# Performance work log

Measured on AMD Instinct MI355X. Metric: run time of the kernel, lower is better.

Reference implementation:

```python
import jax, jax.numpy as jnp
import numpy as np

LATENT = 256; INPUT = 128; NUNITS = 256; DEC_OUT = 128
NTRAJ = 256; NTP = 512
INTERP = 2  # hard-coded in the original forward

def _mlp_sig(x, w1, b1, w2, b2):
    return jax.nn.sigmoid(jnp.tanh(x @ w1 + b1) @ w2 + b2)

def _mlp_lin(x, w1, b1, w2, b2):
    return jnp.tanh(x @ w1 + b1) @ w2 + b2

def _gru_step(y, yt, x, ug, ugt, rg, ns):
    # x: [N, 2*INPUT]; first half = features, second half = observation mask channels
    xh = x[:, :INPUT]
    yc = jnp.concatenate([y, xh], axis=-1)                 # [N, LATENT+INPUT]
    u = _mlp_sig(yc, *ug)
    ut = _mlp_sig(yc, *ugt)
    r = _mlp_sig(yc, *rg)
    new_state = _mlp_lin(jnp.concatenate([y * r, xh], axis=-1), *ns)
    new_y = (1.0 - u) * new_state + u * y
    new_yt = (1.0 - ut) * new_state + ut * yt
    mask = (jnp.sum(x[:, INPUT:], axis=-1, keepdims=True) > 0).astype(x.dtype)
    return mask * new_y + (1.0 - mask) * y, mask * new_yt + (1.0 - mask) * yt

def setup_inputs():
    key = jax.random.key(0)
    ks = iter(jax.random.split(key, 32))
    def p(shape):
        return jax.random.normal(next(ks), shape, dtype=jnp.float32) * 0.05
    d = {}
    d["data"] = jax.random.normal(next(ks), (NTRAJ, NTP, 2 * INPUT), dtype=jnp.float32)
    dts = jax.random.uniform(next(ks), (NTRAJ, NTP), dtype=jnp.float32) + 0.1
    d["time_steps"] = jnp.cumsum(dts, axis=1)              # strictly increasing times
    gin = LATENT + INPUT
    for name in ("ug", "ugt", "rg", "rgt", "ns"):
        d[name + "_w1"] = p((gin, NUNITS)); d[name + "_b1"] = jnp.zeros((NUNITS,), jnp.float32)
        d[name + "_w2"] = p((NUNITS, LATENT)); d[name + "_b2"] = jnp.zeros((LATENT,), jnp.float32)
    d["dk_w1"] = p((LATENT, LATENT)); d["dk_b1"] = jnp.zeros((LATENT,), jnp.float32)
    d["dk_w2"] = p((LATENT, 1)); d["dk_b2"] = jnp.zeros((1,), jnp.float32)
    d["dec_w"] = p((LATENT, DEC_OUT)); d["dec_b"] = jnp.zeros((DEC_OUT,), jnp.float32)
    return d

def reference(data, time_steps,
              ug_w1, ug_b1, ug_w2, ug_b2,
              ugt_w1, ugt_b1, ugt_w2, ugt_b2,
              rg_w1, rg_b1, rg_w2, rg_b2,
              rgt_w1, rgt_b1, rgt_w2, rgt_b2,
              ns_w1, ns_b1, ns_w2, ns_b2,
              dk_w1, dk_b1, dk_w2, dk_b2,
              dec_w, dec_b):
    # Note: reset_gate_target (rgt_*) is computed but never used in the original forward.
    ug = (ug_w1, ug_b1, ug_w2, ug_b2)
    ugt = (ugt_w1, ugt_b1, ugt_w2, ugt_b2)
    rg = (rg_w1, rg_b1, rg_w2, rg_b2)
    ns = (ns_w1, ns_b1, ns_w2, ns_b2)
    n_traj = data.shape[0]
    lin = jnp.linspace(0.0, 1.0, INTERP + 1, dtype=data.dtype)  # [3]
    y0 = jnp.zeros((n_traj, LATENT), data.dtype)
    # step i=0: no decay interpolation, yi_decay = prev_y (zeros)
    y, yt = _gru_step(y0, y0, data[:, 0, :], ug, ugt, rg, ns)
    dts = time_steps[:, 1:] - time_steps[:, :-1]                # [N, T-1]
    xs = jnp.moveaxis(data[:, 1:, :], 1, 0)                     # [T-1, N, 2I]

    def step(carry, inp):
        y, yt = carry
        x, dt = inp
        decay = jax.nn.relu(jax.nn.relu(y @ dk_w1 + dk_b1) @ dk_w2 + dk_b2)  # [N,1]
        e = jnp.exp(-decay * (dt[:, None] * lin[None, :]))                   # [N,3]
        ydec = yt[:, None, :] + (y - yt)[:, None, :] * e[:, :, None]         # [N,3,L]
        vol = jnp.mean(ydec[:, :-1, :] @ dec_w + dec_b, axis=-2)             # [N,D]
        y2, yt2 = _gru_step(ydec[:, -1, :], yt, x, ug, ugt, rg, ns)
        return (y2, yt2), vol

    (y, yt), vols = jax.lax.scan(step, (y, yt), (xs, dts.T))
    prev_y = y[None, :, :]                       # [1, N, L]
    volume_dt = jnp.transpose(vols, (1, 0, 2))   # [N, T-1, D]
    return prev_y, volume_dt, dts
```

## Files before the change

### kernel.cpp

```cpp
#include <hip/hip_runtime.h>
#include <hip/hip_fp16.h>

#define NTRAJ   256
#define NTP     512
#define NSTEPS  511
#define LATENT  256
#define INPUT   128
#define DEC_OUT 128

#define OUT_VOL ((size_t)NTRAJ * LATENT)
#define OUT_DTS (OUT_VOL + (size_t)NTRAJ * NSTEPS * DEC_OUT)

#define WU_UG1  0
#define WU_UG2  49152
#define WU_UGT1 81920
#define WU_UGT2 131072
#define WU_RG1  163840
#define WU_RG2  212992
#define WU_NS1  245760
#define WU_NS2  294912
#define WU_DK1  327680
#define WU_DEC  360448
#define WU_TOT  376832

typedef _Float16 h2_t __attribute__((ext_vector_type(2)));
union U32H2 { unsigned int u; h2_t h; };

__device__ __forceinline__ float dot2f(unsigned int wu, unsigned int xu, float acc) {
#if defined(__has_builtin) && __has_builtin(__builtin_amdgcn_fdot2)
    U32H2 a, b; a.u = wu; b.u = xu;
    return __builtin_amdgcn_fdot2(a.h, b.h, acc, false);
#else
    U32H2 a, b; a.u = wu; b.u = xu;
    return acc + (float)a.h.x * (float)b.h.x + (float)a.h.y * (float)b.h.y;
#endif
}

__device__ __forceinline__ float wred(float v) {
    #pragma unroll
    for (int off = 32; off; off >>= 1) v += __shfl_down(v, off, 64);
    return v;
}
__device__ __forceinline__ float fast_sigmoid(float x) { return 1.0f / (1.0f + __expf(-x)); }
__device__ __forceinline__ float fast_tanh(float x) {
    float e = __expf(2.0f * x);
    return 1.0f - 2.0f / (e + 1.0f);
}
__device__ __forceinline__ unsigned int packpair(float v) {
    float vn = __shfl_xor(v, 1, 64);
    U32H2 r; r.h.x = (_Float16)v; r.h.y = (_Float16)vn;
    return r.u;
}

extern "C" __global__ void __launch_bounds__(256)
convert_w(const float* __restrict__ ug_w1, const float* __restrict__ ug_w2,
          const float* __restrict__ ugt_w1, const float* __restrict__ ugt_w2,
          const float* __restrict__ rg_w1, const float* __restrict__ rg_w2,
          const float* __restrict__ ns_w1, const float* __restrict__ ns_w2,
          const float* __restrict__ dk_w1, const float* __restrict__ dec_w,
          unsigned int* __restrict__ ws)
{
    const int i = blockIdx.x * 256 + threadIdx.x;
    const float* s; int o; int cbits;
    if      (i < WU_UG2)  { s = ug_w1;  o = i;           cbits = 8; }
    else if (i < WU_UGT1) { s = ug_w2;  o = i - WU_UG2;  cbits = 8; }
    else if (i < WU_UGT2) { s = ugt_w1; o = i - WU_UGT1; cbits = 8; }
    else if (i < WU_RG1)  { s = ugt_w2; o = i - WU_UGT2; cbits = 8; }
    else if (i < WU_RG2)  { s = rg_w1;  o = i - WU_RG1;  cbits = 8; }
    else if (i < WU_NS1)  { s = rg_w2;  o = i - WU_RG2;  cbits = 8; }
    else if (i < WU_NS2)  { s = ns_w1;  o = i - WU_NS1;  cbits = 8; }
    else if (i < WU_DK1)  { s = ns_w2;  o = i - WU_NS2;  cbits = 8; }
    else if (i < WU_DEC)  { s = dk_w1;  o = i - WU_DK1;  cbits = 8; }
    else                  { s = dec_w;  o = i - WU_DEC;  cbits = 7; }
    const int C  = 1 << cbits;
    const int kp = o >> cbits;
    const int c  = o & (C - 1);
    const float v0 = s[(2 * kp) * C + c];
    const float v1 = s[(2 * kp + 1) * C + c];
    const unsigned int h0 = __half_as_ushort(__float2half(v0));
    const unsigned int h1 = __half_as_ushort(__float2half(v1));
    ws[i] = h0 | (h1 << 16);
}

#define DOT1(acc, wv, xv) { \
    acc.x = dot2f((wv).x, (xv), acc.x); acc.y = dot2f((wv).y, (xv), acc.y); \
    acc.z = dot2f((wv).z, (xv), acc.z); acc.w = dot2f((wv).w, (xv), acc.w); }

extern "C" __global__ void __launch_bounds__(1024, 4)
rnn_decay_kernel7(const float* __restrict__ data, const float* __restrict__ ts,
                  const float* __restrict__ ug_b1, const float* __restrict__ ug_b2,
                  const float* __restrict__ ugt_b1, const float* __restrict__ ugt_b2,
                  const float* __restrict__ rg_b1, const float* __restrict__ rg_b2,
                  const float* __restrict__ ns_b1, const float* __restrict__ ns_b2,
                  const float* __restrict__ dk_b1, const float* __restrict__ dk_w2,
                  const float* __restrict__ dk_b2, const float* __restrict__ dec_b,
                  const unsigned int* __restrict__ wsu, float* __restrict__ out)
{
    __shared__ __align__(16) float s_part[12288];
    __shared__ __align__(16) float s_partd[4096];
    __shared__ __align__(16) unsigned int s_in_h[192];
    __shared__ __align__(16) unsigned int s_ns_h[192];
    __shared__ __align__(16) unsigned int s_y_h[128];
    __shared__ __align__(16) unsigned int s_a_h[128];
    __shared__ __align__(16) unsigned int s_b_h[128];
    __shared__ __align__(16) unsigned int s_c_h[128];
    __shared__ __align__(16) unsigned int s_v_h[128];
    __shared__ float s_ut[256];
    __shared__ float s_red[8];

    const int tid  = threadIdx.x;
    const int w    = tid >> 6;
    const int lane = tid & 63;
    const int c    = tid & 255;
    const int cl4  = lane << 2;
    const int traj = blockIdx.x;

    const unsigned int* UG1  = wsu + WU_UG1;  const unsigned int* UG2  = wsu + WU_UG2;
    const unsigned int* UGT1 = wsu + WU_UGT1; const unsigned int* UGT2 = wsu + WU_UGT2;
    const unsigned int* RG1  = wsu + WU_RG1;  const unsigned int* RG2  = wsu + WU_RG2;
    const unsigned int* NS1  = wsu + WU_NS1;  const unsigned int* NS2  = wsu + WU_NS2;
    const unsigned int* DK1  = wsu + WU_DK1;  const unsigned int* DECW = wsu + WU_DEC;

    const float* dbase = data + (size_t)traj * NTP * (2 * INPUT);
    const float* tbase = ts + (size_t)traj * NTP;
    float* vol_out = out + OUT_VOL + (size_t)traj * NSTEPS * DEC_OUT;
    float* dts_out = out + OUT_DTS + (size_t)traj * NSTEPS;

    if (tid < 256)
        for (int t0 = c; t0 < NSTEPS; t0 += 256)
            dts_out[t0] = tbase[t0 + 1] - tbase[t0];

    float r_y = 0.f, r_yt = 0.f;

    const int kp12 = w * 12;
    const int kp8  = w << 3;

    for (int t = -1; t < NSTEPS; ++t) {
        const bool first = (t < 0);

        if (tid < 256) {
            const float xval = first ? dbase[c] : dbase[(size_t)(t + 1) * 256 + c];
            float mv = (c >= 128) ? xval : 0.f;
            mv = wred(mv);
            if (lane == 0) s_red[w] = mv;
            if (c < 128) {
                const unsigned int px = packpair(xval);
                if (!(lane & 1)) { s_in_h[128 + (c >> 1)] = px; s_ns_h[128 + (c >> 1)] = px; }
            }
            if (first && !(lane & 1)) s_in_h[c >> 1] = 0u;
        }

        float r_ydec = 0.f, r_u = 0.f;
        bool maskv;

        if (!first) {
            {
                float4 aD = make_float4(0.f, 0.f, 0.f, 0.f);
                #pragma unroll 4
                for (int i = 0; i < 8; ++i) {
                    const int kp = kp8 + i;
                    const unsigned int xv = s_y_h[kp];
                    const uint4 wv = *(const uint4*)(DK1 + (size_t)kp * 256 + cl4);
                    DOT1(aD, wv, xv);
                }
                *(float4*)(s_part + (w << 8) + cl4) = aD;
            }
            __syncthreads();
            if (tid < 256) {
                float v = dk_b1[c];
                #pragma unroll
                for (int i = 0; i < 16; ++i) v += s_part[(i << 8) + c];
                v = fmaxf(v, 0.f);
                const float pv = wred(v * dk_w2[c]);
                if (lane == 0) s_red[4 + w] = pv;
            }
            __syncthreads();
            maskv = (s_red[0] + s_red[1] + s_red[2] + s_red[3]) > 0.f;
            if (tid < 256) {
                const float decay = fmaxf(s_red[4] + s_red[5] + s_red[6] + s_red[7]
                                        + dk_b2[0], 0.f);
                const float dt = tbase[t + 1] - tbase[t];
                const float diff = r_y - r_yt;
                const float ef = __expf(-decay * dt);
                const float eh = __expf(-0.5f * decay * dt);
                r_ydec = r_yt + diff * ef;
                const float vol = 0.5f * (r_y + r_yt + diff * eh);
                const unsigned int pd  = packpair(r_ydec);
                const unsigned int pvv = packpair(vol);
                if (!(lane & 1)) { s_in_h[c >> 1] = pd; s_v_h[c >> 1] = pvv; }
            }
            __syncthreads();
        } else {
            __syncthreads();
            maskv = (s_red[0] + s_red[1] + s_red[2] + s_red[3]) > 0.f;
        }

        if (!first) {
            float4 aE = make_float4(0.f, 0.f, 0.f, 0.f);
            const int hh = lane >> 5, cl = (lane & 31) << 2;
            const int kpb = kp8 + hh;
            #pragma unroll
            for (int i = 0; i < 4; ++i) {
                const int kp = kpb + (i << 1);
                const uint4 wv = *(const uint4*)(DECW + (size_t)kp * 128 + cl);
                const unsigned int xv = s_v_h[kp];
                DOT1(aE, wv, xv);
            }
            *(float4*)(s_partd + ((w << 1) + hh) * 128 + cl) = aE;
        }

        {
            float4 aA = make_float4(0.f, 0.f, 0.f, 0.f), aB = aA, aC = aA;
            #pragma unroll 4
            for (int i = 0; i < 12; ++i) {
                const int kp = kp12 + i;
                const unsigned int xv = s_in_h[kp];
                const uint4 wa = *(const uint4*)(UG1  + (size_t)kp * 256 + cl4);
                const uint4 wb = *(const uint4*)(UGT1 + (size_t)kp * 256 + cl4);
                const uint4 wc = *(const uint4*)(RG1  + (size_t)kp * 256 + cl4);
                DOT1(aA, wa, xv); DOT1(aB, wb, xv); DOT1(aC, wc, xv);
            }
            *(float4*)(s_part + (w << 8) + cl4)          = aA;
            *(float4*)(s_part + 4096 + (w << 8) + cl4)   = aB;
            *(float4*)(s_part + 8192 + (w << 8) + cl4)   = aC;
        }
        __syncthreads();
        {
            const int s = tid >> 8;
            if (s == 0) {
                float v = ug_b1[c];
                #pragma unroll
                for (int i = 0; i < 16; ++i) v += s_part[(i << 8) + c];
                v = fast_tanh(v);
                const unsigned int pk = packpair(v);
                if (!(lane & 1)) s_a_h[c >> 1] = pk;
            } else if (s == 1) {
                float v = ugt_b1[c];
                #pragma unroll
                for (int i = 0; i < 16; ++i) v += s_part[4096 + (i << 8) + c];
                v = fast_tanh(v);
                const unsigned int pk = packpair(v);
                if (!(lane & 1)) s_b_h[c >> 1] = pk;
            } else if (s == 2) {
                float v = rg_b1[c];
                #pragma unroll
                for (int i = 0; i < 16; ++i) v += s_part[8192 + (i << 8) + c];
                v = fast_tanh(v);
                const unsigned int pk = packpair(v);
                if (!(lane & 1)) s_c_h[c >> 1] = pk;
            } else if (!first && c < 128) {
                float vd = dec_b[c];
                #pragma unroll
                for (int i = 0; i < 32; ++i) vd += s_partd[(i << 7) + c];
                vol_out[(size_t)t * DEC_OUT + c] = vd;
            }
        }
        __syncthreads();

        {
            float4 aA = make_float4(0.f, 0.f, 0.f, 0.f), aB = aA, aC = aA;
            #pragma unroll 4
            for (int i = 0; i < 8; ++i) {
                const int kp = kp8 + i;
                const unsigned int xa = s_a_h[kp];
                const unsigned int xb = s_b_h[kp];
                const unsigned int xc = s_c_h[kp];
                const uint4 wa = *(const uint4*)(UG2  + (size_t)kp * 256 + cl4);
                const uint4 wb = *(const uint4*)(UGT2 + (size_t)kp * 256 + cl4);
                const uint4 wc = *(const uint4*)(RG2  + (size_t)kp * 256 + cl4);
                DOT1(aA, wa, xa); DOT1(aB, wb, xb); DOT1(aC, wc, xc);
            }
            *(float4*)(s_part + (w << 8) + cl4)          = aA;
            *(float4*)(s_part + 4096 + (w << 8) + cl4)   = aB;
            *(float4*)(s_part + 8192 + (w << 8) + cl4)   = aC;
        }
        __syncthreads();
        {
            const int s = tid >> 8;
            if (s == 0) {
                float v = ug_b2[c];
                #pragma unroll
                for (int i = 0; i < 16; ++i) v += s_part[(i << 8) + c];
                r_u = fast_sigmoid(v);
                float v2 = rg_b2[c];
                #pragma unroll
                for (int i = 0; i < 16; ++i) v2 += s_part[8192 + (i << 8) + c];
                const float rr = fast_sigmoid(v2);
                const unsigned int pk = packpair(r_ydec * rr);
                if (!(lane & 1)) s_ns_h[c >> 1] = pk;
            } else if (s == 1) {
                float v = ugt_b2[c];
                #pragma unroll
                for (int i = 0; i < 16; ++i) v += s_part[4096 + (i << 8) + c];
                s_ut[c] = fast_sigmoid(v);
            }
        }
        __syncthreads();

        {
            float4 aA = make_float4(0.f, 0.f, 0.f, 0.f);
            #pragma unroll 4
            for (int i = 0; i < 12; ++i) {
                const int kp = kp12 + i;
                const unsigned int xv = s_ns_h[kp];
                const uint4 wa = *(const uint4*)(NS1 + (size_t)kp * 256 + cl4);
                DOT1(aA, wa, xv);
            }
            *(float4*)(s_part + (w << 8) + cl4) = aA;
        }
        __syncthreads();
        if (tid < 256) {
            float v = ns_b1[c];
            #pragma unroll
            for (int i = 0; i < 16; ++i) v += s_part[(i << 8) + c];
            v = fast_tanh(v);
            const unsigned int pk = packpair(v);
            if (!(lane & 1)) s_a_h[c >> 1] = pk;
        }
        __syncthreads();

        {
            float4 aA = make_float4(0.f, 0.f, 0.f, 0.f);
            #pragma unroll 4
            for (int i = 0; i < 8; ++i) {
                const int kp = kp8 + i;
                const unsigned int xv = s_a_h[kp];
                const uint4 wa = *(const uint4*)(NS2 + (size_t)kp * 256 + cl4);
                DOT1(aA, wa, xv);
            }
            *(float4*)(s_part + (w << 8) + cl4) = aA;
        }
        __syncthreads();
        if (tid < 256) {
            float nsv = ns_b2[c];
            #pragma unroll
            for (int i = 0; i < 16; ++i) nsv += s_part[(i << 8) + c];
            const float u = r_u, ut = s_ut[c];
            const float ny  = (1.f - u)  * nsv + u  * r_ydec;
            const float nyt = (1.f - ut) * nsv + ut * r_yt;
            r_y  = maskv ? ny  : r_ydec;
            r_yt = maskv ? nyt : r_yt;
            const unsigned int pk = packpair(r_y);
            if (!(lane & 1)) s_y_h[c >> 1] = pk;
        }
        __syncthreads();
    }

    if (tid < 256)
        out[(size_t)traj * 256 + c] = r_y;
}

extern "C" void kernel_launch(void* const* d_in, const int* in_sizes, int n_in,
                              void* d_out, int out_size, void* d_ws, size_t ws_size,
                              hipStream_t stream) {
    const float* data   = (const float*)d_in[0];
    const float* ts     = (const float*)d_in[1];
    const float* ug_w1  = (const float*)d_in[2];
    const float* ug_b1  = (const float*)d_in[3];
    const float* ug_w2  = (const float*)d_in[4];
    const float* ug_b2  = (const float*)d_in[5];
    const float* ugt_w1 = (const float*)d_in[6];
    const float* ugt_b1 = (const float*)d_in[7];
    const float* ugt_w2 = (const float*)d_in[8];
    const float* ugt_b2 = (const float*)d_in[9];
    const float* rg_w1  = (const float*)d_in[10];
    const float* rg_b1  = (const float*)d_in[11];
    const float* rg_w2  = (const float*)d_in[12];
    const float* rg_b2  = (const float*)d_in[13];
    const float* ns_w1  = (const float*)d_in[18];
    const float* ns_b1  = (const float*)d_in[19];
    const float* ns_w2  = (const float*)d_in[20];
    const float* ns_b2  = (const float*)d_in[21];
    const float* dk_w1  = (const float*)d_in[22];
    const float* dk_b1  = (const float*)d_in[23];
    const float* dk_w2  = (const float*)d_in[24];
    const float* dk_b2  = (const float*)d_in[25];
    const float* dec_w  = (const float*)d_in[26];
    const float* dec_b  = (const float*)d_in[27];

    unsigned int* wsu = (unsigned int*)d_ws;

    convert_w<<<WU_TOT / 256, 256, 0, stream>>>(ug_w1, ug_w2, ugt_w1, ugt_w2,
                                                rg_w1, rg_w2, ns_w1, ns_w2,
                                                dk_w1, dec_w, wsu);

    rnn_decay_kernel7<<<NTRAJ, 1024, 0, stream>>>(
        data, ts, ug_b1, ug_b2, ugt_b1, ugt_b2, rg_b1, rg_b2, ns_b1, ns_b2,
        dk_b1, dk_w2, dk_b2, dec_b, wsu, (float*)d_out);
}
```

Measured before the change: 7.624 ms.

## Process two trajectories per block to share weight loads across trajectories

```diff
diff --git a/kernel.cpp b/kernel.cpp
--- a/kernel.cpp
+++ b/kernel.cpp
@@ -86,8 +86,8 @@
     acc.x = dot2f((wv).x, (xv), acc.x); acc.y = dot2f((wv).y, (xv), acc.y); \
     acc.z = dot2f((wv).z, (xv), acc.z); acc.w = dot2f((wv).w, (xv), acc.w); }
 
-extern "C" __global__ void __launch_bounds__(1024, 4)
-rnn_decay_kernel7(const float* __restrict__ data, const float* __restrict__ ts,
+extern "C" __global__ void __launch_bounds__(512, 2)
+rnn_decay_kernel8(const float* __restrict__ data, const float* __restrict__ ts,
                   const float* __restrict__ ug_b1, const float* __restrict__ ug_b2,
                   const float* __restrict__ ugt_b1, const float* __restrict__ ugt_b2,
                   const float* __restrict__ rg_b1, const float* __restrict__ rg_b2,
@@ -96,24 +96,24 @@
                   const float* __restrict__ dk_b2, const float* __restrict__ dec_b,
                   const unsigned int* __restrict__ wsu, float* __restrict__ out)
 {
-    __shared__ __align__(16) float s_part[12288];
-    __shared__ __align__(16) float s_partd[4096];
-    __shared__ __align__(16) unsigned int s_in_h[192];
-    __shared__ __align__(16) unsigned int s_ns_h[192];
-    __shared__ __align__(16) unsigned int s_y_h[128];
-    __shared__ __align__(16) unsigned int s_a_h[128];
-    __shared__ __align__(16) unsigned int s_b_h[128];
-    __shared__ __align__(16) unsigned int s_c_h[128];
-    __shared__ __align__(16) unsigned int s_v_h[128];
-    __shared__ float s_ut[256];
-    __shared__ float s_red[8];
+    __shared__ __align__(16) float s_part[2][8192];
+    __shared__ __align__(16) unsigned int s_in_h[2][192];
+    __shared__ __align__(16) unsigned int s_ns_h[2][192];
+    __shared__ __align__(16) unsigned int s_y_h[2][128];
+    __shared__ __align__(16) unsigned int s_a_h[2][128];
+    __shared__ __align__(16) unsigned int s_b_h[2][128];
+    __shared__ __align__(16) unsigned int s_c_h[2][128];
+    __shared__ __align__(16) unsigned int s_v_h[2][128];
+    __shared__ float s_red[2][8];
 
     const int tid  = threadIdx.x;
     const int w    = tid >> 6;
     const int lane = tid & 63;
     const int c    = tid & 255;
+    const int h    = tid >> 8;
+    const int wg   = w & 3;
     const int cl4  = lane << 2;
-    const int traj = blockIdx.x;
+    const int traj = (blockIdx.x << 1) + h;
 
     const unsigned int* UG1  = wsu + WU_UG1;  const unsigned int* UG2  = wsu + WU_UG2;
     const unsigned int* UGT1 = wsu + WU_UGT1; const unsigned int* UGT2 = wsu + WU_UGT2;
@@ -126,59 +126,60 @@
     float* vol_out = out + OUT_VOL + (size_t)traj * NSTEPS * DEC_OUT;
     float* dts_out = out + OUT_DTS + (size_t)traj * NSTEPS;
 
-    if (tid < 256)
-        for (int t0 = c; t0 < NSTEPS; t0 += 256)
-            dts_out[t0] = tbase[t0 + 1] - tbase[t0];
+    for (int t0 = c; t0 < NSTEPS; t0 += 256)
+        dts_out[t0] = tbase[t0 + 1] - tbase[t0];
 
     float r_y = 0.f, r_yt = 0.f;
 
-    const int kp12 = w * 12;
-    const int kp8  = w << 3;
+    const int kp24 = w * 24;
+    const int kp16 = w << 4;
 
     for (int t = -1; t < NSTEPS; ++t) {
         const bool first = (t < 0);
 
-        if (tid < 256) {
+        {
             const float xval = first ? dbase[c] : dbase[(size_t)(t + 1) * 256 + c];
             float mv = (c >= 128) ? xval : 0.f;
             mv = wred(mv);
-            if (lane == 0) s_red[w] = mv;
+            if (lane == 0) s_red[h][wg] = mv;
             if (c < 128) {
                 const unsigned int px = packpair(xval);
-                if (!(lane & 1)) { s_in_h[128 + (c >> 1)] = px; s_ns_h[128 + (c >> 1)] = px; }
-            }
-            if (first && !(lane & 1)) s_in_h[c >> 1] = 0u;
-        }
-
-        float r_ydec = 0.f, r_u = 0.f;
+                if (!(lane & 1)) { s_in_h[h][128 + (c >> 1)] = px; s_ns_h[h][128 + (c >> 1)] = px; }
+            }
+            if (first && !(lane & 1)) s_in_h[h][c >> 1] = 0u;
+        }
+
+        float r_ydec = 0.f, r_u = 0.f, r_ut = 0.f;
         bool maskv;
 
         if (!first) {
             {
-                float4 aD = make_float4(0.f, 0.f, 0.f, 0.f);
+                float4 a0 = make_float4(0.f, 0.f, 0.f, 0.f), a1 = a0;
                 #pragma unroll 4
-                for (int i = 0; i < 8; ++i) {
-                    const int kp = kp8 + i;
-                    const unsigned int xv = s_y_h[kp];
+                for (int i = 0; i < 16; ++i) {
+                    const int kp = kp16 + i;
+                    const unsigned int x0 = s_y_h[0][kp];
+                    const unsigned int x1 = s_y_h[1][kp];
                     const uint4 wv = *(const uint4*)(DK1 + (size_t)kp * 256 + cl4);
-                    DOT1(aD, wv, xv);
+                    DOT1(a0, wv, x0); DOT1(a1, wv, x1);
                 }
-                *(float4*)(s_part + (w << 8) + cl4) = aD;
+                *(float4*)(&s_part[0][(w << 8) + cl4]) = a0;
+                *(float4*)(&s_part[1][(w << 8) + cl4]) = a1;
             }
             __syncthreads();
-            if (tid < 256) {
+            {
                 float v = dk_b1[c];
                 #pragma unroll
-                for (int i = 0; i < 16; ++i) v += s_part[(i << 8) + c];
+                for (int i = 0; i < 8; ++i) v += s_part[h][(i << 8) + c];
                 v = fmaxf(v, 0.f);
                 const float pv = wred(v * dk_w2[c]);
-                if (lane == 0) s_red[4 + w] = pv;
+                if (lane == 0) s_red[h][4 + wg] = pv;
             }
             __syncthreads();
-            maskv = (s_red[0] + s_red[1] + s_red[2] + s_red[3]) > 0.f;
-            if (tid < 256) {
-                const float decay = fmaxf(s_red[4] + s_red[5] + s_red[6] + s_red[7]
-                                        + dk_b2[0], 0.f);
+            maskv = (s_red[h][0] + s_red[h][1] + s_red[h][2] + s_red[h][3]) > 0.f;
+            {
+                const float decay = fmaxf(s_red[h][4] + s_red[h][5] + s_red[h][6]
+                                        + s_red[h][7] + dk_b2[0], 0.f);
                 const float dt = tbase[t + 1] - tbase[t];
                 const float diff = r_y - r_yt;
                 const float ef = __expf(-decay * dt);
@@ -187,167 +188,177 @@
                 const float vol = 0.5f * (r_y + r_yt + diff * eh);
                 const unsigned int pd  = packpair(r_ydec);
                 const unsigned int pvv = packpair(vol);
-                if (!(lane & 1)) { s_in_h[c >> 1] = pd; s_v_h[c >> 1] = pvv; }
+                if (!(lane & 1)) { s_in_h[h][c >> 1] = pd; s_v_h[h][c >> 1] = pvv; }
             }
             __syncthreads();
         } else {
             __syncthreads();
-            maskv = (s_red[0] + s_red[1] + s_red[2] + s_red[3]) > 0.f;
+            maskv = (s_red[h][0] + s_red[h][1] + s_red[h][2] + s_red[h][3]) > 0.f;
         }
 
         if (!first) {
-            float4 aE = make_float4(0.f, 0.f, 0.f, 0.f);
+            float4 e0 = make_float4(0.f, 0.f, 0.f, 0.f), e1 = e0;
             const int hh = lane >> 5, cl = (lane & 31) << 2;
-            const int kpb = kp8 + hh;
-            #pragma unroll
-            for (int i = 0; i < 4; ++i) {
+            const int kpb = kp16 + hh;
+            #pragma unroll 4
+            for (int i = 0; i < 8; ++i) {
                 const int kp = kpb + (i << 1);
                 const uint4 wv = *(const uint4*)(DECW + (size_t)kp * 128 + cl);
-                const unsigned int xv = s_v_h[kp];
-                DOT1(aE, wv, xv);
-            }
-            *(float4*)(s_partd + ((w << 1) + hh) * 128 + cl) = aE;
-        }
-
-        {
-            float4 aA = make_float4(0.f, 0.f, 0.f, 0.f), aB = aA, aC = aA;
+                const unsigned int x0 = s_v_h[0][kp];
+                const unsigned int x1 = s_v_h[1][kp];
+                DOT1(e0, wv, x0); DOT1(e1, wv, x1);
+            }
+            const int slot = 6144 + ((w << 1) + hh) * 128 + cl;
+            *(float4*)(&s_part[0][slot]) = e0;
+            *(float4*)(&s_part[1][slot]) = e1;
+        }
+
+        {
+            float4 aA0 = make_float4(0.f, 0.f, 0.f, 0.f), aB0 = aA0, aC0 = aA0;
+            float4 aA1 = aA0, aB1 = aA0, aC1 = aA0;
             #pragma unroll 4
-            for (int i = 0; i < 12; ++i) {
-                const int kp = kp12 + i;
-                const unsigned int xv = s_in_h[kp];
+            for (int i = 0; i < 24; ++i) {
+                const int kp = kp24 + i;
+                const unsigned int x0 = s_in_h[0][kp];
+                const unsigned int x1 = s_in_h[1][kp];
                 const uint4 wa = *(const uint4*)(UG1  + (size_t)kp * 256 + cl4);
                 const uint4 wb = *(const uint4*)(UGT1 + (size_t)kp * 256 + cl4);
                 const uint4 wc = *(const uint4*)(RG1  + (size_t)kp * 256 + cl4);
-                DOT1(aA, wa, xv); DOT1(aB, wb, xv); DOT1(aC, wc, xv);
-            }
-            *(float4*)(s_part + (w << 8) + cl4)          = aA;
-            *(float4*)(s_part + 4096 + (w << 8) + cl4)   = aB;
-            *(float4*)(s_part + 8192 + (w << 8) + cl4)   = aC;
-        }
-        __syncthreads();
-        {
-            const int s = tid >> 8;
-            if (s == 0) {
-                float v = ug_b1[c];
-                #pragma unroll
-                for (int i = 0; i < 16; ++i) v += s_part[(i << 8) + c];
-                v = fast_tanh(v);
-                const unsigned int pk = packpair(v);
-                if (!(lane & 1)) s_a_h[c >> 1] = pk;
-            } else if (s == 1) {
-                float v = ugt_b1[c];
-                #pragma unroll
-                for (int i = 0; i < 16; ++i) v += s_part[4096 + (i << 8) + c];
-                v = fast_tanh(v);
-                const unsigned int pk = packpair(v);
-                if (!(lane & 1)) s_b_h[c >> 1] = pk;
-            } else if (s == 2) {
-                float v = rg_b1[c];
-                #pragma unroll
-                for (int i = 0; i < 16; ++i) v += s_part[8192 + (i << 8) + c];
-                v = fast_tanh(v);
-                const unsigned int pk = packpair(v);
-                if (!(lane & 1)) s_c_h[c >> 1] = pk;
-            } else if (!first && c < 128) {
+                DOT1(aA0, wa, x0); DOT1(aA1, wa, x1);
+                DOT1(aB0, wb, x0); DOT1(aB1, wb, x1);
+                DOT1(aC0, wc, x0); DOT1(aC1, wc, x1);
+            }
+            *(float4*)(&s_part[0][(w << 8) + cl4])        = aA0;
+            *(float4*)(&s_part[0][2048 + (w << 8) + cl4]) = aB0;
+            *(float4*)(&s_part[0][4096 + (w << 8) + cl4]) = aC0;
+            *(float4*)(&s_part[1][(w << 8) + cl4])        = aA1;
+            *(float4*)(&s_part[1][2048 + (w << 8) + cl4]) = aB1;
+            *(float4*)(&s_part[1][4096 + (w << 8) + cl4]) = aC1;
+        }
+        __syncthreads();
+        {
+            float v = ug_b1[c];
+            #pragma unroll
+            for (int i = 0; i < 8; ++i) v += s_part[h][(i << 8) + c];
+            v = fast_tanh(v);
+            const unsigned int pka = packpair(v);
+            if (!(lane & 1)) s_a_h[h][c >> 1] = pka;
+            float v2 = ugt_b1[c];
+            #pragma unroll
+            for (int i = 0; i < 8; ++i) v2 += s_part[h][2048 + (i << 8) + c];
+            v2 = fast_tanh(v2);
+            const unsigned int pkb = packpair(v2);
+            if (!(lane & 1)) s_b_h[h][c >> 1] = pkb;
+            float v3 = rg_b1[c];
+            #pragma unroll
+            for (int i = 0; i < 8; ++i) v3 += s_part[h][4096 + (i << 8) + c];
+            v3 = fast_tanh(v3);
+            const unsigned int pkc = packpair(v3);
+            if (!(lane & 1)) s_c_h[h][c >> 1] = pkc;
+            if (!first && c < 128) {
                 float vd = dec_b[c];
                 #pragma unroll
-                for (int i = 0; i < 32; ++i) vd += s_partd[(i << 7) + c];
+                for (int i = 0; i < 16; ++i) vd += s_part[h][6144 + (i << 7) + c];
                 vol_out[(size_t)t * DEC_OUT + c] = vd;
             }
         }
         __syncthreads();
 
         {
-            float4 aA = make_float4(0.f, 0.f, 0.f, 0.f), aB = aA, aC = aA;
+            float4 aA0 = make_float4(0.f, 0.f, 0.f, 0.f), aB0 = aA0, aC0 = aA0;
+            float4 aA1 = aA0, aB1 = aA0, aC1 = aA0;
             #pragma unroll 4
-            for (int i = 0; i < 8; ++i) {
-                const int kp = kp8 + i;
-                const unsigned int xa = s_a_h[kp];
-                const unsigned int xb = s_b_h[kp];
-                const unsigned int xc = s_c_h[kp];
+            for (int i = 0; i < 16; ++i) {
+                const int kp = kp16 + i;
+                const unsigned int xa0 = s_a_h[0][kp], xa1 = s_a_h[1][kp];
+                const unsigned int xb0 = s_b_h[0][kp], xb1 = s_b_h[1][kp];
+                const unsigned int xc0 = s_c_h[0][kp], xc1 = s_c_h[1][kp];
                 const uint4 wa = *(const uint4*)(UG2  + (size_t)kp * 256 + cl4);
                 const uint4 wb = *(const uint4*)(UGT2 + (size_t)kp * 256 + cl4);
                 const uint4 wc = *(const uint4*)(RG2  + (size_t)kp * 256 + cl4);
-                DOT1(aA, wa, xa); DOT1(aB, wb, xb); DOT1(aC, wc, xc);
-            }
-            *(float4*)(s_part + (w << 8) + cl4)          = aA;
-            *(float4*)(s_part + 4096 + (w << 8) + cl4)   = aB;
-            *(float4*)(s_part + 8192 + (w << 8) + cl4)   = aC;
-        }
-        __syncthreads();
-        {
-            const int s = tid >> 8;
-            if (s == 0) {
-                float v = ug_b2[c];
-                #pragma unroll
-                for (int i = 0; i < 16; ++i) v += s_part[(i << 8) + c];
-                r_u = fast_sigmoid(v);
-                float v2 = rg_b2[c];
-                #pragma unroll
-                for (int i = 0; i < 16; ++i) v2 += s_part[8192 + (i << 8) + c];
-                const float rr = fast_sigmoid(v2);
-                const unsigned int pk = packpair(r_ydec * rr);
-                if (!(lane & 1)) s_ns_h[c >> 1] = pk;
-            } else if (s == 1) {
-                float v = ugt_b2[c];
-                #pragma unroll
-                for (int i = 0; i < 16; ++i) v += s_part[4096 + (i << 8) + c];
-                s_ut[c] = fast_sigmoid(v);
-            }
-        }
-        __syncthreads();
-
-        {
-            float4 aA = make_float4(0.f, 0.f, 0.f, 0.f);
+                DOT1(aA0, wa, xa0); DOT1(aA1, wa, xa1);
+                DOT1(aB0, wb, xb0); DOT1(aB1, wb, xb1);
+                DOT1(aC0, wc, xc0); DOT1(aC1, wc, xc1);
+            }
+            *(float4*)(&s_part[0][(w << 8) + cl4])        = aA0;
+            *(float4*)(&s_part[0][2048 + (w << 8) + cl4]) = aB0;
+            *(float4*)(&s_part[0][4096 + (w << 8) + cl4]) = aC0;
+            *(float4*)(&s_part[1][(w << 8) + cl4])        = aA1;
+            *(float4*)(&s_part[1][2048 + (w << 8) + cl4]) = aB1;
+            *(float4*)(&s_part[1][4096 + (w << 8) + cl4]) = aC1;
+        }
+        __syncthreads();
+        {
+            float v = ug_b2[c];
+            #pragma unroll
+            for (int i = 0; i < 8; ++i) v += s_part[h][(i << 8) + c];
+            r_u = fast_sigmoid(v);
+            float v2 = ugt_b2[c];
+            #pragma unroll
+            for (int i = 0; i < 8; ++i) v2 += s_part[h][2048 + (i << 8) + c];
+            r_ut = fast_sigmoid(v2);
+            float v3 = rg_b2[c];
+            #pragma unroll
+            for (int i = 0; i < 8; ++i) v3 += s_part[h][4096 + (i << 8) + c];
+            const float rr = fast_sigmoid(v3);
+            const unsigned int pk = packpair(r_ydec * rr);
+            if (!(lane & 1)) s_ns_h[h][c >> 1] = pk;
+        }
+        __syncthreads();
+
+        {
+            float4 a0 = make_float4(0.f, 0.f, 0.f, 0.f), a1 = a0;
             #pragma unroll 4
-            for (int i = 0; i < 12; ++i) {
-                const int kp = kp12 + i;
-                const unsigned int xv = s_ns_h[kp];
+            for (int i = 0; i < 24; ++i) {
+                const int kp = kp24 + i;
+                const unsigned int x0 = s_ns_h[0][kp];
+                const unsigned int x1 = s_ns_h[1][kp];
                 const uint4 wa = *(const uint4*)(NS1 + (size_t)kp * 256 + cl4);
-                DOT1(aA, wa, xv);
-            }
-            *(float4*)(s_part + (w << 8) + cl4) = aA;
-        }
-        __syncthreads();
-        if (tid < 256) {
+                DOT1(a0, wa, x0); DOT1(a1, wa, x1);
+            }
+            *(float4*)(&s_part[0][(w << 8) + cl4]) = a0;
+            *(float4*)(&s_part[1][(w << 8) + cl4]) = a1;
+        }
+        __syncthreads();
+        {
             float v = ns_b1[c];
             #pragma unroll
-            for (int i = 0; i < 16; ++i) v += s_part[(i << 8) + c];
+            for (int i = 0; i < 8; ++i) v += s_part[h][(i << 8) + c];
             v = fast_tanh(v);
             const unsigned int pk = packpair(v);
-            if (!(lane & 1)) s_a_h[c >> 1] = pk;
-        }
-        __syncthreads();
-
-        {
-            float4 aA = make_float4(0.f, 0.f, 0.f, 0.f);
+            if (!(lane & 1)) s_a_h[h][c >> 1] = pk;
+        }
+        __syncthreads();
+
+        {
+            float4 a0 = make_float4(0.f, 0.f, 0.f, 0.f), a1 = a0;
             #pragma unroll 4
-            for (int i = 0; i < 8; ++i) {
-                const int kp = kp8 + i;
-                const unsigned int xv = s_a_h[kp];
+            for (int i = 0; i < 16; ++i) {
+                const int kp = kp16 + i;
+                const unsigned int x0 = s_a_h[0][kp];
+                const unsigned int x1 = s_a_h[1][kp];
                 const uint4 wa = *(const uint4*)(NS2 + (size_t)kp * 256 + cl4);
-                DOT1(aA, wa, xv);
-            }
-            *(float4*)(s_part + (w << 8) + cl4) = aA;
-        }
-        __syncthreads();
-        if (tid < 256) {
+                DOT1(a0, wa, x0); DOT1(a1, wa, x1);
+            }
+            *(float4*)(&s_part[0][(w << 8) + cl4]) = a0;
+            *(float4*)(&s_part[1][(w << 8) + cl4]) = a1;
+        }
+        __syncthreads();
+        {
             float nsv = ns_b2[c];
             #pragma unroll
-            for (int i = 0; i < 16; ++i) nsv += s_part[(i << 8) + c];
-            const float u = r_u, ut = s_ut[c];
-            const float ny  = (1.f - u)  * nsv + u  * r_ydec;
-            const float nyt = (1.f - ut) * nsv + ut * r_yt;
+            for (int i = 0; i < 8; ++i) nsv += s_part[h][(i << 8) + c];
+            const float ny  = (1.f - r_u)  * nsv + r_u  * r_ydec;
+            const float nyt = (1.f - r_ut) * nsv + r_ut * r_yt;
             r_y  = maskv ? ny  : r_ydec;
             r_yt = maskv ? nyt : r_yt;
             const unsigned int pk = packpair(r_y);
-            if (!(lane & 1)) s_y_h[c >> 1] = pk;
+            if (!(lane & 1)) s_y_h[h][c >> 1] = pk;
         }
         __syncthreads();
     }
 
-    if (tid < 256)
-        out[(size_t)traj * 256 + c] = r_y;
+    out[(size_t)traj * 256 + c] = r_y;
 }
 
 extern "C" void kernel_launch(void* const* d_in, const int* in_sizes, int n_in,
@@ -384,7 +395,7 @@
                                                 rg_w1, rg_w2, ns_w1, ns_w2,
                                                 dk_w1, dec_w, wsu);
 
-    rnn_decay_kernel7<<<NTRAJ, 1024, 0, stream>>>(
+    rnn_decay_kernel8<<<NTRAJ / 2, 512, 0, stream>>>(
         data, ts, ug_b1, ug_b2, ugt_b1, ugt_b2, rg_b1, rg_b2, ns_b1, ns_b2,
         dk_b1, dk_w2, dk_b2, dec_b, wsu, (float*)d_out);
 }
```

Measured after the change: 7.773 ms. No clear change (+2.0%).
